# Kernel optimization log

Hardware: AMD Instinct MI355X
Metric: run time of the kernel (lower is better)

Reference implementation:

```python
import jax, jax.numpy as jnp
from jax import lax
import numpy as np

EMBED = 1024
HIDDEN = 1024
VOCAB = 32000
T = 64


def setup_inputs() -> dict:
    key = jax.random.key(0)
    ks = jax.random.split(key, 8)
    s = 0.02  # weight init scale
    return {
        "captions": jax.random.randint(ks[0], (T,), 0, VOCAB, dtype=jnp.int32),
        "features": jax.random.normal(ks[1], (EMBED,), dtype=jnp.float32),
        "embed_table": jax.random.normal(ks[2], (VOCAB, EMBED), dtype=jnp.float32) * s,
        "W_ih": jax.random.normal(ks[3], (4 * HIDDEN, EMBED), dtype=jnp.float32) * s,
        "W_hh": jax.random.normal(ks[4], (4 * HIDDEN, HIDDEN), dtype=jnp.float32) * s,
        "b_ih": jnp.zeros((4 * HIDDEN,), dtype=jnp.float32),
        "b_hh": jnp.zeros((4 * HIDDEN,), dtype=jnp.float32),
        "fc_W": jax.random.normal(ks[5], (VOCAB, HIDDEN), dtype=jnp.float32) * s,
        "fc_b": jnp.zeros((VOCAB,), dtype=jnp.float32),
    }


def reference(captions, features, embed_table, W_ih, W_hh, b_ih, b_hh, fc_W, fc_b):
    # Embedding lookup for all caption tokens: [T, E]
    emb = embed_table[captions]
    # Input at t=0 is the visual feature; at t>0 it is embed(captions[t-1]).
    xs = jnp.concatenate([features[None, :], emb[:-1]], axis=0)  # [T, E]
    H = W_hh.shape[1]
    bias = b_ih + b_hh  # fuse the two LSTMCell biases

    def step(carry, x):
        h, c = carry  # [H], [H]  (batch = 1, kept 1-D)
        gates = x @ W_ih.T + h @ W_hh.T + bias  # [4H]
        i, f, g, o = jnp.split(gates, 4)  # PyTorch gate order: i, f, g, o
        i = jax.nn.sigmoid(i)
        f = jax.nn.sigmoid(f)
        g = jnp.tanh(g)
        o = jax.nn.sigmoid(o)
        c = f * c + i * g
        h = o * jnp.tanh(c)
        return (h, c), h

    h0 = jnp.zeros((H,), dtype=features.dtype)
    (_, _), hs = lax.scan(step, (h0, h0), xs)  # hs: [T, H]
    # Per-step Linear, expressed as one batched GEMM over all timesteps.
    logits = hs @ fc_W.T + fc_b  # [T, V]
    return logits[None, :, :]  # [1, T, V] to match outputs[:, t, :]
```

## Files before the change

kernel.cpp:

```cpp
#include <hip/hip_runtime.h>
#include <hip/hip_cooperative_groups.h>
#include <math.h>

namespace cg = cooperative_groups;

#define EMBED  1024
#define HIDDEN 1024
#define VOCAB  32000
#define TSTEPS 64
#define G4     4096
#define NBLK   256

__global__ void build_xs(const int* __restrict__ caps,
                         const float* __restrict__ feat,
                         const float* __restrict__ table,
                         float* __restrict__ xs) {
    int t = blockIdx.x;
    int e = threadIdx.x + blockIdx.y * 256;
    float v;
    if (t == 0) {
        v = feat[e];
    } else {
        size_t row = (size_t)caps[t - 1];
        v = table[row * EMBED + e];
    }
    xs[(size_t)t * EMBED + e] = v;
}

__global__ __launch_bounds__(256) void xg_gemm(const float* __restrict__ xs,
                                               const float* __restrict__ Wih,
                                               const float* __restrict__ bih,
                                               const float* __restrict__ bhh,
                                               float* __restrict__ Xg) {
    __shared__ float xs_s[64][132];
    int tid = threadIdx.x;
    int jl  = tid & 15;
    int tg  = tid >> 4;
    int j   = blockIdx.x * 16 + jl;
    const float* wrow = Wih + (size_t)j * EMBED;
    float acc[4] = {0.f, 0.f, 0.f, 0.f};

    for (int c = 0; c < 8; ++c) {
        __syncthreads();
        for (int idx = tid; idx < 64 * 32; idx += 256) {
            int r = idx >> 5, f4 = idx & 31;
            float4 v = ((const float4*)(xs + (size_t)r * EMBED + c * 128))[f4];
            *((float4*)&xs_s[r][f4 * 4]) = v;
        }
        __syncthreads();
        for (int f4 = 0; f4 < 32; ++f4) {
            float4 w = ((const float4*)(wrow + c * 128))[f4];
#pragma unroll
            for (int k = 0; k < 4; ++k) {
                const float* xr = &xs_s[tg * 4 + k][f4 * 4];
                acc[k] += w.x * xr[0] + w.y * xr[1] + w.z * xr[2] + w.w * xr[3];
            }
        }
    }
    float bias = bih[j] + bhh[j];
#pragma unroll
    for (int k = 0; k < 4; ++k) {
        Xg[(size_t)(tg * 4 + k) * G4 + j] = acc[k] + bias;
    }
}

__global__ __launch_bounds__(256, 1) void lstm_seq(const float* __restrict__ Xg,
                                                   const float* __restrict__ Whh,
                                                   unsigned long long* hbuf,
                                                   float* __restrict__ hs) {
    __shared__ float h_s[2][HIDDEN];
    __shared__ float xg_s[TSTEPS][16];

    int tid  = threadIdx.x;
    int lane = tid & 63;
    int wv   = tid >> 6;
    int g    = lane >> 4;
    int c16  = lane & 15;
    int q0   = blockIdx.x * 4;
    int hj   = q0 + wv;
    const float4* wrow = (const float4*)(Whh + ((size_t)g * HIDDEN + hj) * HIDDEN);

    float4 wreg[16];
#pragma unroll
    for (int k = 0; k < 16; ++k) wreg[k] = wrow[c16 + 16 * k];

    for (int idx = tid; idx < TSTEPS * 16; idx += 256) {
        int t = idx >> 4, r = idx & 15, gg = r >> 2, w = r & 3;
        xg_s[t][r] = Xg[(size_t)t * G4 + gg * HIDDEN + q0 + w];
    }

    float cstate = 0.0f;

    for (int t = 0; t < TSTEPS; ++t) {
        unsigned long long* hsrc = hbuf + (size_t)(t & 1) * HIDDEN;
        unsigned tag = (unsigned)t;
        float* dst = h_s[t & 1];

        unsigned long long x0 = 0, x1 = 0, x2 = 0, x3 = 0;
        int need = 0xF;
        do {
            if (need & 1) {
                x0 = __hip_atomic_load(hsrc + tid, __ATOMIC_RELAXED,
                                       __HIP_MEMORY_SCOPE_AGENT);
                if ((unsigned)(x0 >> 32) == tag) need &= ~1;
            }
            if (need & 2) {
                x1 = __hip_atomic_load(hsrc + tid + 256, __ATOMIC_RELAXED,
                                       __HIP_MEMORY_SCOPE_AGENT);
                if ((unsigned)(x1 >> 32) == tag) need &= ~2;
            }
            if (need & 4) {
                x2 = __hip_atomic_load(hsrc + tid + 512, __ATOMIC_RELAXED,
                                       __HIP_MEMORY_SCOPE_AGENT);
                if ((unsigned)(x2 >> 32) == tag) need &= ~4;
            }
            if (need & 8) {
                x3 = __hip_atomic_load(hsrc + tid + 768, __ATOMIC_RELAXED,
                                       __HIP_MEMORY_SCOPE_AGENT);
                if ((unsigned)(x3 >> 32) == tag) need &= ~8;
            }
            if (need) __builtin_amdgcn_s_sleep(1);
        } while (need);
        dst[tid]       = __uint_as_float((unsigned)x0);
        dst[tid + 256] = __uint_as_float((unsigned)x1);
        dst[tid + 512] = __uint_as_float((unsigned)x2);
        dst[tid + 768] = __uint_as_float((unsigned)x3);
        __syncthreads();

        float4 a = {0.f, 0.f, 0.f, 0.f};
#pragma unroll
        for (int k = 0; k < 16; ++k) {
            float4 w = wreg[k];
            const float* hv = &dst[(c16 + 16 * k) * 4];
            a.x += w.x * hv[0];
            a.y += w.y * hv[1];
            a.z += w.z * hv[2];
            a.w += w.w * hv[3];
        }
        float sum = (a.x + a.y) + (a.z + a.w);
        sum += __shfl_xor(sum, 1);
        sum += __shfl_xor(sum, 2);
        sum += __shfl_xor(sum, 4);
        sum += __shfl_xor(sum, 8);
        float s0 = __shfl(sum, 0);
        float s1 = __shfl(sum, 16);
        float s2 = __shfl(sum, 32);
        float s3 = __shfl(sum, 48);

        if (lane == 0) {
            float gi = s0 + xg_s[t][wv];
            float gf = s1 + xg_s[t][4 + wv];
            float gg = s2 + xg_s[t][8 + wv];
            float go = s3 + xg_s[t][12 + wv];
            float i_ = 1.f / (1.f + expf(-gi));
            float f_ = 1.f / (1.f + expf(-gf));
            float g_ = tanhf(gg);
            float o_ = 1.f / (1.f + expf(-go));
            cstate = f_ * cstate + i_ * g_;
            float hv = o_ * tanhf(cstate);
            unsigned long long pk =
                ((unsigned long long)(unsigned)(t + 1) << 32) |
                (unsigned long long)__float_as_uint(hv);
            __hip_atomic_store(hbuf + (size_t)((t + 1) & 1) * HIDDEN + hj, pk,
                               __ATOMIC_RELAXED, __HIP_MEMORY_SCOPE_AGENT);
            hs[(size_t)t * HIDDEN + hj] = hv;
        }
    }
}

__global__ __launch_bounds__(256) void logits_gemm(const float* __restrict__ hs,
                                                   const float* __restrict__ fcW,
                                                   const float* __restrict__ fcb,
                                                   float* __restrict__ out) {
    __shared__ float hs_s[64][132];
    int tid = threadIdx.x;
    int vl  = tid & 31;
    int tg  = tid >> 5;
    int v   = blockIdx.x * 32 + vl;
    const float* wrow = fcW + (size_t)v * HIDDEN;
    float acc[8] = {0.f, 0.f, 0.f, 0.f, 0.f, 0.f, 0.f, 0.f};

    for (int c = 0; c < 8; ++c) {
        __syncthreads();
        for (int idx = tid; idx < 64 * 32; idx += 256) {
            int r = idx >> 5, f4 = idx & 31;
            float4 h4 = ((const float4*)(hs + (size_t)r * HIDDEN + c * 128))[f4];
            *((float4*)&hs_s[r][f4 * 4]) = h4;
        }
        __syncthreads();
        for (int f4 = 0; f4 < 32; ++f4) {
            float4 w = ((const float4*)(wrow + c * 128))[f4];
#pragma unroll
            for (int k = 0; k < 8; ++k) {
                const float* hv = &hs_s[tg * 8 + k][f4 * 4];
                acc[k] += w.x * hv[0] + w.y * hv[1] + w.z * hv[2] + w.w * hv[3];
            }
        }
    }
    float b = fcb[v];
#pragma unroll
    for (int k = 0; k < 8; ++k) {
        out[(size_t)(tg * 8 + k) * VOCAB + v] = acc[k] + b;
    }
}

extern "C" void kernel_launch(void* const* d_in, const int* in_sizes, int n_in,
                              void* d_out, int out_size, void* d_ws, size_t ws_size,
                              hipStream_t stream) {
    const int*   caps  = (const int*)  d_in[0];
    const float* feat  = (const float*)d_in[1];
    const float* table = (const float*)d_in[2];
    const float* Wih   = (const float*)d_in[3];
    const float* Whh   = (const float*)d_in[4];
    const float* bih   = (const float*)d_in[5];
    const float* bhh   = (const float*)d_in[6];
    const float* fcW   = (const float*)d_in[7];
    const float* fcb   = (const float*)d_in[8];
    float* out = (float*)d_out;

    char* ws = (char*)d_ws;
    float* xs = (float*)(ws);
    float* Xg = (float*)(ws + 262144);
    float* hs = (float*)(ws + 262144 + 1048576);
    unsigned long long* hbuf =
        (unsigned long long*)(ws + 262144 + 1048576 + 262144);

    hipMemsetAsync(hbuf, 0, 2 * HIDDEN * sizeof(unsigned long long), stream);

    build_xs<<<dim3(TSTEPS, 4), 256, 0, stream>>>(caps, feat, table, xs);
    xg_gemm <<<256, 256, 0, stream>>>(xs, Wih, bih, bhh, Xg);

    void* args[] = {(void*)&Xg, (void*)&Whh, (void*)&hbuf, (void*)&hs};
    hipLaunchCooperativeKernel(lstm_seq, dim3(NBLK), dim3(256), args, 0u, stream);

    logits_gemm<<<VOCAB / 32, 256, 0, stream>>>(hs, fcW, fcb, out);
}
```

Baseline: 675.0 us.

## Stage weight tiles in LDS and register-block the logits GEMM

Both the input-gate GEMM and the vocabulary-projection GEMM now load weight rows cooperatively into shared memory with coalesced float4 reads. Before, each thread streamed its own strided weight row from global memory. The logits kernel also switches to a 4x4 register tile per thread with 64 vocab rows per block, which raises reuse of each loaded value. The LDS row stride is now an odd 133 floats, meant to cut bank conflicts. That stride leaves float4 LDS accesses misaligned, which may split them into slower accesses.

New measurement: 650.9 us. 3.6% less time.

```diff
diff --git a/kernel.cpp b/kernel.cpp
--- a/kernel.cpp
+++ b/kernel.cpp
@@ -10,6 +10,7 @@
 #define TSTEPS 64
 #define G4     4096
 #define NBLK   256
+#define RS     133
 
 __global__ void build_xs(const int* __restrict__ caps,
                          const float* __restrict__ feat,
@@ -32,12 +33,13 @@
                                                const float* __restrict__ bih,
                                                const float* __restrict__ bhh,
                                                float* __restrict__ Xg) {
-    __shared__ float xs_s[64][132];
+    __shared__ float xs_s[64][RS];
+    __shared__ float w_s[16][RS];
     int tid = threadIdx.x;
     int jl  = tid & 15;
     int tg  = tid >> 4;
-    int j   = blockIdx.x * 16 + jl;
-    const float* wrow = Wih + (size_t)j * EMBED;
+    int j0  = blockIdx.x * 16;
+    int j   = j0 + jl;
     float acc[4] = {0.f, 0.f, 0.f, 0.f};
 
     for (int c = 0; c < 8; ++c) {
@@ -47,9 +49,14 @@
             float4 v = ((const float4*)(xs + (size_t)r * EMBED + c * 128))[f4];
             *((float4*)&xs_s[r][f4 * 4]) = v;
         }
+        for (int idx = tid; idx < 16 * 32; idx += 256) {
+            int r = idx >> 5, f4 = idx & 31;
+            float4 v = ((const float4*)(Wih + (size_t)(j0 + r) * EMBED + c * 128))[f4];
+            *((float4*)&w_s[r][f4 * 4]) = v;
+        }
         __syncthreads();
         for (int f4 = 0; f4 < 32; ++f4) {
-            float4 w = ((const float4*)(wrow + c * 128))[f4];
+            float4 w = *((const float4*)&w_s[jl][f4 * 4]);
 #pragma unroll
             for (int k = 0; k < 4; ++k) {
                 const float* xr = &xs_s[tg * 4 + k][f4 * 4];
@@ -172,13 +179,19 @@
                                                    const float* __restrict__ fcW,
                                                    const float* __restrict__ fcb,
                                                    float* __restrict__ out) {
-    __shared__ float hs_s[64][132];
+    __shared__ float hs_s[64][RS];
+    __shared__ float w_s[64][RS];
     int tid = threadIdx.x;
-    int vl  = tid & 31;
-    int tg  = tid >> 5;
-    int v   = blockIdx.x * 32 + vl;
-    const float* wrow = fcW + (size_t)v * HIDDEN;
-    float acc[8] = {0.f, 0.f, 0.f, 0.f, 0.f, 0.f, 0.f, 0.f};
+    int tv  = tid & 15;
+    int tg  = tid >> 4;
+    int j0  = tv * 4;
+    int i0  = tg * 4;
+    int v0  = blockIdx.x * 64;
+    float acc[4][4];
+#pragma unroll
+    for (int i = 0; i < 4; ++i)
+#pragma unroll
+        for (int j = 0; j < 4; ++j) acc[i][j] = 0.f;
 
     for (int c = 0; c < 8; ++c) {
         __syncthreads();
@@ -187,20 +200,35 @@
             float4 h4 = ((const float4*)(hs + (size_t)r * HIDDEN + c * 128))[f4];
             *((float4*)&hs_s[r][f4 * 4]) = h4;
         }
+        for (int idx = tid; idx < 64 * 32; idx += 256) {
+            int r = idx >> 5, f4 = idx & 31;
+            float4 w4 = ((const float4*)(fcW + (size_t)(v0 + r) * HIDDEN + c * 128))[f4];
+            *((float4*)&w_s[r][f4 * 4]) = w4;
+        }
         __syncthreads();
         for (int f4 = 0; f4 < 32; ++f4) {
-            float4 w = ((const float4*)(wrow + c * 128))[f4];
-#pragma unroll
-            for (int k = 0; k < 8; ++k) {
-                const float* hv = &hs_s[tg * 8 + k][f4 * 4];
-                acc[k] += w.x * hv[0] + w.y * hv[1] + w.z * hv[2] + w.w * hv[3];
-            }
-        }
-    }
-    float b = fcb[v];
-#pragma unroll
-    for (int k = 0; k < 8; ++k) {
-        out[(size_t)(tg * 8 + k) * VOCAB + v] = acc[k] + b;
+            float4 wv[4], hv[4];
+#pragma unroll
+            for (int j = 0; j < 4; ++j) wv[j] = *((const float4*)&w_s[j0 + j][f4 * 4]);
+#pragma unroll
+            for (int i = 0; i < 4; ++i) hv[i] = *((const float4*)&hs_s[i0 + i][f4 * 4]);
+#pragma unroll
+            for (int i = 0; i < 4; ++i)
+#pragma unroll
+                for (int j = 0; j < 4; ++j) {
+                    acc[i][j] += wv[j].x * hv[i].x + wv[j].y * hv[i].y +
+                                 wv[j].z * hv[i].z + wv[j].w * hv[i].w;
+                }
+        }
+    }
+    float b0 = fcb[v0 + j0 + 0];
+    float b1 = fcb[v0 + j0 + 1];
+    float b2 = fcb[v0 + j0 + 2];
+    float b3 = fcb[v0 + j0 + 3];
+#pragma unroll
+    for (int i = 0; i < 4; ++i) {
+        float4 o = {acc[i][0] + b0, acc[i][1] + b1, acc[i][2] + b2, acc[i][3] + b3};
+        *((float4*)&out[(size_t)(i0 + i) * VOCAB + v0 + j0]) = o;
     }
 }
 
@@ -233,5 +261,5 @@
     void* args[] = {(void*)&Xg, (void*)&Whh, (void*)&hbuf, (void*)&hs};
     hipLaunchCooperativeKernel(lstm_seq, dim3(NBLK), dim3(256), args, 0u, stream);
 
-    logits_gemm<<<VOCAB / 32, 256, 0, stream>>>(hs, fcW, fcb, out);
-}
+    logits_gemm<<<VOCAB / 64, 256, 0, stream>>>(hs, fcW, fcb, out);
+}
```
